# Performance work log

Measured on AMD Instinct MI355X. Metric: run time of the kernel, lower is better.

## Reference

```python
import jax, jax.numpy as jnp
import numpy as np
from jax.scipy.special import gammaln

RES = 512    # init res
STEPS = 128  # init steps


def setup_inputs() -> dict:
    key = jax.random.key(0)
    # control points in [0,1]^2: [batch, n_strks, n_points, 2]
    control_points = jax.random.uniform(key, (16, 4, 4, 2), dtype=jnp.float32)
    sigma = jnp.float32(0.02)  # Gaussian kernel bandwidth
    return {"control_points": control_points, "sigma": sigma}


def _bernstein(order, n_steps):
    # feat[k, t] = C(order, k) * t**(order-k) * (1-t)**k, matching sample_curve
    t = jnp.linspace(0.0, 1.0, n_steps, dtype=jnp.float32)          # [T]
    k = jnp.arange(order + 1, dtype=jnp.float32)[:, None]           # [K,1]
    o = jnp.float32(order)
    log_comb = gammaln(o + 1.0) - gammaln(k + 1.0) - gammaln(o - k + 1.0)
    return jnp.exp(log_comb) * t[None, :] ** (o - k) * (1.0 - t[None, :]) ** k  # [K,T]


def reference(control_points, sigma):
    """Bezier.forward with method='base', keep_strk_dim=True.
    Returns [batch, n_strks, 1, res, res]."""
    b, s, n_pts, _ = control_points.shape
    feat = _bernstein(n_pts - 1, STEPS)                              # [K,T]
    curve = jnp.einsum('bcki,kt->bcit', control_points, feat)       # [b,s,2,T]
    x = curve[:, :, 0]                                               # [b,s,T]
    y = curve[:, :, 1]                                               # [b,s,T]
    g = jnp.arange(RES, dtype=jnp.float32) / RES                     # pixel coords
    inv = 1.0 / (2.0 * sigma ** 2)
    # Gaussian splat is separable: exp(-(dx^2+dy^2)/2s^2) = exp(-dx^2/2s^2)*exp(-dy^2/2s^2)
    # raster[b,s,p,q] = sum_t Ay[b,s,t,p] * Ax[b,s,t,q]  (x indexes columns q, y rows p,
    # matching torch meshgrid + transpose(1,3) layout)
    Ax = jnp.exp(-(x[..., None] - g) ** 2 * inv)                     # [b,s,T,res]
    Ay = jnp.exp(-(y[..., None] - g) ** 2 * inv)                     # [b,s,T,res]
    raster = jnp.einsum('bstp,bstq->bspq', Ay, Ax)                   # [b,s,res,res]
    return raster[:, :, None]                                        # [b,s,1,res,res]
```

## Files before the change

### kernel.cpp

```cpp
#include <hip/hip_runtime.h>
#include <math.h>

#define RES   512
#define STEPS 128
#define BH    8

__global__ __launch_bounds__(256) void bezier_rows_kernel(
    const float* __restrict__ cp,
    const float* __restrict__ sigma_ptr,
    float* __restrict__ out)
{
    __shared__ float xc[STEPS];
    __shared__ float yc[STEPS];
    __shared__ float ayc[STEPS][BH];
    __shared__ int   nact_s;

    const int img = blockIdx.y;
    const int p0  = blockIdx.x * BH;
    const int tid = threadIdx.x;

    const float sigma = sigma_ptr[0];
    const float inv   = 1.0f / (2.0f * sigma * sigma);
    const float msq   = 16.0f / inv;
    const float margin = sqrtf(msq);

    if (tid == 0) nact_s = 0;
    __syncthreads();

    if (tid < STEPS) {
        const float w  = (float)tid * (1.0f / 127.0f);
        const float v  = 1.0f - w;
        const float b0 = w * w * w;
        const float b1 = 3.0f * w * w * v;
        const float b2 = 3.0f * w * v * v;
        const float b3 = v * v * v;
        const float* c = cp + (size_t)img * 8;
        const float x = c[0]*b0 + c[2]*b1 + c[4]*b2 + c[6]*b3;
        const float y = c[1]*b0 + c[3]*b1 + c[5]*b2 + c[7]*b3;
        const float lo = (float)p0          * (1.0f / RES) - margin;
        const float hi = (float)(p0 + BH-1) * (1.0f / RES) + margin;
        if (y >= lo && y <= hi) {
            const int s = atomicAdd(&nact_s, 1);
            xc[s] = x;
            yc[s] = y;
        }
    }
    __syncthreads();
    const int nact = nact_s;

    for (int e = tid; e < nact * BH; e += 256) {
        const int s = e >> 3;
        const int i = e & (BH - 1);
        const float dy = yc[s] - (float)(p0 + i) * (1.0f / RES);
        ayc[s][i] = __expf(-dy * dy * inv);
    }
    __syncthreads();

    float acc0[BH] = {0.f,0.f,0.f,0.f,0.f,0.f,0.f,0.f};
    float acc1[BH] = {0.f,0.f,0.f,0.f,0.f,0.f,0.f,0.f};
    const float gq0 = (float)tid         * (1.0f / RES);
    const float gq1 = (float)(tid + 256) * (1.0f / RES);

    for (int s = 0; s < nact; ++s) {
        const float xv  = xc[s];
        const float dx0 = xv - gq0;
        const float dx1 = xv - gq1;
        const int h0 = __any(dx0 * dx0 < msq);
        const int h1 = __any(dx1 * dx1 < msq);
        if (!(h0 | h1)) continue;
        const float4 a0 = *(const float4*)&ayc[s][0];
        const float4 a1 = *(const float4*)&ayc[s][4];
        if (h0) {
            const float ax = __expf(-dx0 * dx0 * inv);
            acc0[0] += ax * a0.x; acc0[1] += ax * a0.y;
            acc0[2] += ax * a0.z; acc0[3] += ax * a0.w;
            acc0[4] += ax * a1.x; acc0[5] += ax * a1.y;
            acc0[6] += ax * a1.z; acc0[7] += ax * a1.w;
        }
        if (h1) {
            const float ax = __expf(-dx1 * dx1 * inv);
            acc1[0] += ax * a0.x; acc1[1] += ax * a0.y;
            acc1[2] += ax * a0.z; acc1[3] += ax * a0.w;
            acc1[4] += ax * a1.x; acc1[5] += ax * a1.y;
            acc1[6] += ax * a1.z; acc1[7] += ax * a1.w;
        }
    }

    #pragma unroll
    for (int i = 0; i < BH; ++i) {
        const size_t rowoff = ((size_t)img * RES + (size_t)(p0 + i)) * RES;
        out[rowoff + tid]       = acc0[i];
        out[rowoff + tid + 256] = acc1[i];
    }
}

extern "C" void kernel_launch(void* const* d_in, const int* in_sizes, int n_in,
                              void* d_out, int out_size, void* d_ws, size_t ws_size,
                              hipStream_t stream) {
    const float* cp    = (const float*)d_in[0];
    const float* sigma = (const float*)d_in[1];
    float* out         = (float*)d_out;
    const int n_img    = in_sizes[0] / 8;
    dim3 grid(RES / BH, n_img);
    bezier_rows_kernel<<<grid, 256, 0, stream>>>(cp, sigma, out);
}
```

Before: 97.30 us.

## Build per-wave column-chunk sample lists and widen row band to sixteen

Each wave now builds a compacted list, using ballot and popcount, of the curve samples whose x lies near its 64-column chunk. The inner loop then iterates only over relevant samples, with no per-sample wave vote or skipped iterations. The row band per block doubles to 16, so each x-Gaussian evaluation is reused across more rows, at the cost of more accumulator registers and half as many blocks. The list-building pass adds shared memory and a small setup cost per block.

```diff
diff --git a/kernel.cpp b/kernel.cpp
--- a/kernel.cpp
+++ b/kernel.cpp
@@ -1,30 +1,35 @@
 #include <hip/hip_runtime.h>
 #include <math.h>
 
-#define RES   512
-#define STEPS 128
-#define BH    8
+#define RES    512
+#define STEPS  128
+#define BH     16
+#define NCHUNK 8
 
-__global__ __launch_bounds__(256) void bezier_rows_kernel(
+__global__ __launch_bounds__(256) void bezier_band_kernel(
     const float* __restrict__ cp,
     const float* __restrict__ sigma_ptr,
     float* __restrict__ out)
 {
-    __shared__ float xc[STEPS];
-    __shared__ float yc[STEPS];
+    __shared__ float xb[STEPS];
+    __shared__ float yb[STEPS];
     __shared__ float ayc[STEPS][BH];
-    __shared__ int   nact_s;
+    __shared__ unsigned char clist[NCHUNK][STEPS];
+    __shared__ int  ccnt[NCHUNK];
+    __shared__ int  nb_s;
 
-    const int img = blockIdx.y;
-    const int p0  = blockIdx.x * BH;
-    const int tid = threadIdx.x;
+    const int img  = blockIdx.y;
+    const int p0   = blockIdx.x * BH;
+    const int tid  = threadIdx.x;
+    const int lane = tid & 63;
+    const int wave = tid >> 6;
 
-    const float sigma = sigma_ptr[0];
-    const float inv   = 1.0f / (2.0f * sigma * sigma);
-    const float msq   = 16.0f / inv;
+    const float sigma  = sigma_ptr[0];
+    const float inv    = 1.0f / (2.0f * sigma * sigma);
+    const float msq    = 16.0f / inv;
     const float margin = sqrtf(msq);
 
-    if (tid == 0) nact_s = 0;
+    if (tid == 0) nb_s = 0;
     __syncthreads();
 
     if (tid < STEPS) {
@@ -37,53 +42,88 @@
         const float* c = cp + (size_t)img * 8;
         const float x = c[0]*b0 + c[2]*b1 + c[4]*b2 + c[6]*b3;
         const float y = c[1]*b0 + c[3]*b1 + c[5]*b2 + c[7]*b3;
-        const float lo = (float)p0          * (1.0f / RES) - margin;
-        const float hi = (float)(p0 + BH-1) * (1.0f / RES) + margin;
+        const float lo = (float)p0            * (1.0f / RES) - margin;
+        const float hi = (float)(p0 + BH - 1) * (1.0f / RES) + margin;
         if (y >= lo && y <= hi) {
-            const int s = atomicAdd(&nact_s, 1);
-            xc[s] = x;
-            yc[s] = y;
+            const int s = atomicAdd(&nb_s, 1);
+            xb[s] = x;
+            yb[s] = y;
         }
     }
     __syncthreads();
-    const int nact = nact_s;
+    const int nb = nb_s;
 
-    for (int e = tid; e < nact * BH; e += 256) {
-        const int s = e >> 3;
+    for (int e = tid; e < nb * BH; e += 256) {
+        const int s = e >> 4;
         const int i = e & (BH - 1);
-        const float dy = yc[s] - (float)(p0 + i) * (1.0f / RES);
+        const float dy = yb[s] - (float)(p0 + i) * (1.0f / RES);
         ayc[s][i] = __expf(-dy * dy * inv);
+    }
+
+    #pragma unroll
+    for (int cc = 0; cc < 2; ++cc) {
+        const int c = wave + 4 * cc;
+        const float lo = (float)(c * 64)      * (1.0f / RES) - margin;
+        const float hi = (float)(c * 64 + 63) * (1.0f / RES) + margin;
+        int cnt = 0;
+        for (int base = 0; base < nb; base += 64) {
+            const int s = base + lane;
+            const bool act = (s < nb) && (xb[s] >= lo) && (xb[s] <= hi);
+            const unsigned long long m = __ballot(act);
+            if (act) {
+                const int pos = __popcll(m & ((1ull << lane) - 1ull));
+                clist[c][cnt + pos] = (unsigned char)s;
+            }
+            cnt += __popcll(m);
+        }
+        if (lane == 0) ccnt[c] = cnt;
     }
     __syncthreads();
 
-    float acc0[BH] = {0.f,0.f,0.f,0.f,0.f,0.f,0.f,0.f};
-    float acc1[BH] = {0.f,0.f,0.f,0.f,0.f,0.f,0.f,0.f};
+    float acc0[BH], acc1[BH];
+    #pragma unroll
+    for (int i = 0; i < BH; ++i) { acc0[i] = 0.0f; acc1[i] = 0.0f; }
+
     const float gq0 = (float)tid         * (1.0f / RES);
     const float gq1 = (float)(tid + 256) * (1.0f / RES);
+    const int c0 = wave;
+    const int c1 = wave + 4;
 
-    for (int s = 0; s < nact; ++s) {
-        const float xv  = xc[s];
-        const float dx0 = xv - gq0;
-        const float dx1 = xv - gq1;
-        const int h0 = __any(dx0 * dx0 < msq);
-        const int h1 = __any(dx1 * dx1 < msq);
-        if (!(h0 | h1)) continue;
+    const int n0 = ccnt[c0];
+    for (int j = 0; j < n0; ++j) {
+        const int   s  = clist[c0][j];
+        const float dx = xb[s] - gq0;
+        const float ax = __expf(-dx * dx * inv);
         const float4 a0 = *(const float4*)&ayc[s][0];
         const float4 a1 = *(const float4*)&ayc[s][4];
-        if (h0) {
-            const float ax = __expf(-dx0 * dx0 * inv);
-            acc0[0] += ax * a0.x; acc0[1] += ax * a0.y;
-            acc0[2] += ax * a0.z; acc0[3] += ax * a0.w;
-            acc0[4] += ax * a1.x; acc0[5] += ax * a1.y;
-            acc0[6] += ax * a1.z; acc0[7] += ax * a1.w;
-        }
-        if (h1) {
-            const float ax = __expf(-dx1 * dx1 * inv);
-            acc1[0] += ax * a0.x; acc1[1] += ax * a0.y;
-            acc1[2] += ax * a0.z; acc1[3] += ax * a0.w;
-            acc1[4] += ax * a1.x; acc1[5] += ax * a1.y;
-            acc1[6] += ax * a1.z; acc1[7] += ax * a1.w;
-        }
+        const float4 a2 = *(const float4*)&ayc[s][8];
+        const float4 a3 = *(const float4*)&ayc[s][12];
+        acc0[0]  += ax * a0.x; acc0[1]  += ax * a0.y;
+        acc0[2]  += ax * a0.z; acc0[3]  += ax * a0.w;
+        acc0[4]  += ax * a1.x; acc0[5]  += ax * a1.y;
+        acc0[6]  += ax * a1.z; acc0[7]  += ax * a1.w;
+        acc0[8]  += ax * a2.x; acc0[9]  += ax * a2.y;
+        acc0[10] += ax * a2.z; acc0[11] += ax * a2.w;
+        acc0[12] += ax * a3.x; acc0[13] += ax * a3.y;
+        acc0[14] += ax * a3.z; acc0[15] += ax * a3.w;
+    }
+    const int n1 = ccnt[c1];
+    for (int j = 0; j < n1; ++j) {
+        const int   s  = clist[c1][j];
+        const float dx = xb[s] - gq1;
+        const float ax = __expf(-dx * dx * inv);
+        const float4 a0 = *(const float4*)&ayc[s][0];
+        const float4 a1 = *(const float4*)&ayc[s][4];
+        const float4 a2 = *(const float4*)&ayc[s][8];
+        const float4 a3 = *(const float4*)&ayc[s][12];
+        acc1[0]  += ax * a0.x; acc1[1]  += ax * a0.y;
+        acc1[2]  += ax * a0.z; acc1[3]  += ax * a0.w;
+        acc1[4]  += ax * a1.x; acc1[5]  += ax * a1.y;
+        acc1[6]  += ax * a1.z; acc1[7]  += ax * a1.w;
+        acc1[8]  += ax * a2.x; acc1[9]  += ax * a2.y;
+        acc1[10] += ax * a2.z; acc1[11] += ax * a2.w;
+        acc1[12] += ax * a3.x; acc1[13] += ax * a3.y;
+        acc1[14] += ax * a3.z; acc1[15] += ax * a3.w;
     }
 
     #pragma unroll
@@ -102,5 +142,5 @@
     float* out         = (float*)d_out;
     const int n_img    = in_sizes[0] / 8;
     dim3 grid(RES / BH, n_img);
-    bezier_rows_kernel<<<grid, 256, 0, stream>>>(cp, sigma, out);
+    bezier_band_kernel<<<grid, 256, 0, stream>>>(cp, sigma, out);
 }
```

After: 92.42 us. 5.0% less time.
